# Performance work log

Measured on AMD Instinct MI355X. Metric: run time of the kernel, lower is better.

The kernel has to match this reference:

```python
import jax, jax.numpy as jnp
import numpy as np

CODEBOOK_SIZE = 1024
LATENT_DIM = 64
BETA = 0.25
DECAY = 0.99
EPS = 1e-05


def _hadamard(n):
    H = np.array([[1.0]], dtype=np.float32)
    while H.shape[0] < n:
        H = np.kron(H, np.array([[1.0, 1.0], [1.0, -1.0]], dtype=np.float32))
    return H


def setup_inputs() -> dict:
    key = jax.random.key(0)
    k1, k2, k3 = jax.random.split(key, 3)
    x = jax.random.normal(k1, (16, LATENT_DIM, 64, 64), dtype=jnp.float32)
    lim = 1.0 / CODEBOOK_SIZE
    embedding_weight = jax.random.uniform(k2, (CODEBOOK_SIZE, LATENT_DIM), jnp.float32, -lim, lim)
    ema_w = jax.random.uniform(k3, (CODEBOOK_SIZE, LATENT_DIM), jnp.float32, -lim, lim)
    ema_cluster_size = jnp.ones((CODEBOOK_SIZE,), jnp.float32)
    rotation_matrix = jnp.asarray(_hadamard(LATENT_DIM))
    return {"x": x, "embedding_weight": embedding_weight, "rotation_matrix": rotation_matrix,
            "ema_cluster_size": ema_cluster_size, "ema_w": ema_w}


def reference(x, embedding_weight, rotation_matrix, ema_cluster_size, ema_w):
    sg = jax.lax.stop_gradient
    B, C, H, W = x.shape
    K, D = embedding_weight.shape
    # [B,C,H,W] -> [N, D]
    x_flat = jnp.transpose(x, (0, 2, 3, 1)).reshape(-1, D)
    x_rot = x_flat @ rotation_matrix
    # squared euclidean distances [N, K]
    dist = (jnp.sum(x_rot * x_rot, axis=-1, keepdims=True)
            + jnp.sum(embedding_weight * embedding_weight, axis=-1)[None, :]
            - 2.0 * (x_rot @ embedding_weight.T))
    idx = jnp.argmin(dist, axis=-1)  # [N]
    quant_flat = embedding_weight[idx]  # gather == one-hot @ E
    quant = jnp.transpose(quant_flat.reshape(B, H, W, C), (0, 3, 1, 2))
    commitment_loss = BETA * jnp.mean((sg(quant) - x) ** 2)
    codebook_loss = jnp.mean((quant - sg(x)) ** 2)
    N = x_flat.shape[0]
    counts = jax.ops.segment_sum(jnp.ones((N,), x.dtype), idx, num_segments=K)
    avg_probs = counts / N
    entropy_loss = -jnp.sum(avg_probs * jnp.log(avg_probs + 1e-10))
    loss = codebook_loss + commitment_loss + entropy_loss
    # EMA bookkeeping (training path; detached in the original)
    new_cs = ema_cluster_size * DECAY + (1.0 - DECAY) * counts
    n_tot = jnp.sum(new_cs)
    new_cs = (new_cs + EPS) / (n_tot + K * EPS) * n_tot
    dw = jax.ops.segment_sum(sg(x_rot), idx, num_segments=K)  # encodings.T @ x_rot
    new_ema_w = ema_w * DECAY + (1.0 - DECAY) * dw
    new_embedding = new_ema_w / new_cs[:, None]
    # straight-through estimator
    quant_out = x + sg(quant - x)
    return quant_out, loss, idx, new_embedding, new_cs, new_ema_w
```

## Files before the change

### kernel.cpp

```cpp
#include <hip/hip_runtime.h>
#include <cmath>

#define PAD 68


__global__ __launch_bounds__(256) void vq_init_kernel(const float* __restrict__ E,
                                                      float* __restrict__ ws) {
    #pragma clang fp contract(off)
    int g = blockIdx.x * 256 + threadIdx.x;
    ws[2048 + g] = 0.0f;
    if (g < 1024) {
        ws[1024 + g] = 0.0f;
        const float* e = E + g * 64;
        float r[8];
        #pragma unroll
        for (int j = 0; j < 8; ++j) r[j] = e[j] * e[j];
        #pragma unroll
        for (int t = 1; t < 8; ++t)
            #pragma unroll
            for (int j = 0; j < 8; ++j) {
                float sq = e[8 * t + j] * e[8 * t + j];
                r[j] = r[j] + sq;
            }
        ws[g] = ((r[0] + r[1]) + (r[2] + r[3])) + ((r[4] + r[5]) + (r[6] + r[7]));
    }
    if (g == 0) ws[67584] = 0.0f;
}

__global__ __launch_bounds__(256, 4) void vq_main_kernel(
    const float* __restrict__ x, const float* __restrict__ E,
    const float* __restrict__ R, float* __restrict__ ws, float* __restrict__ out)
{
    #pragma clang fp contract(off)
    __shared__ float s_A[64][PAD];
    __shared__ float s_B[64][PAD];
    __shared__ float s_ee[64];
    __shared__ float s_xx[64];
    __shared__ int   s_idx[64];
    __shared__ float s_red[8];

    const int tid = threadIdx.x;
    const int tc = tid >> 4;
    const int tr = tid & 15;
    const int brow = blockIdx.x;
    const int b = brow >> 6, h = brow & 63;

    const float* ee_g  = ws;
    float* counts  = ws + 1024;
    float* dw      = ws + 2048;
    float* mse_acc = ws + 67584;
    float* out_q   = out;
    float* out_idx = out + 4194305;

    const size_t xbase = (size_t)b * 262144 + (size_t)h * 64;

    #pragma unroll
    for (int i = 0; i < 4; ++i) {
        int d  = i * 16 + (tid >> 4);
        int w4 = (tid & 15) * 4;
        float4 v = *(const float4*)(x + xbase + (size_t)d * 4096 + w4);
        *(float4*)&s_A[d][w4] = v;
        float4 r = *(const float4*)(R + d * 64 + w4);
        *(float4*)&s_B[d][w4] = r;
    }
    __syncthreads();

    {
        float acc[4][4] = {};
        for (int d = 0; d < 64; ++d) {
            float xv[4], rv[4];
            #pragma unroll
            for (int i = 0; i < 4; ++i) xv[i] = s_A[d][tc + 16 * i];
            #pragma unroll
            for (int j = 0; j < 4; ++j) rv[j] = s_B[d][tr + 16 * j];
            #pragma unroll
            for (int i = 0; i < 4; ++i)
                #pragma unroll
                for (int j = 0; j < 4; ++j)
                    acc[i][j] = fmaf(xv[i], rv[j], acc[i][j]);
        }
        __syncthreads();
        #pragma unroll
        for (int i = 0; i < 4; ++i)
            #pragma unroll
            for (int j = 0; j < 4; ++j)
                s_B[tc + 16 * i][tr + 16 * j] = acc[i][j];
    }
    __syncthreads();

    if (tid < 64) {
        const int w = tid;
        float r[8];
        #pragma unroll
        for (int j = 0; j < 8; ++j) { float u = s_B[w][j]; r[j] = u * u; }
        #pragma unroll
        for (int t = 1; t < 8; ++t)
            #pragma unroll
            for (int j = 0; j < 8; ++j) {
                float u = s_B[w][8 * t + j];
                float sq = u * u;
                r[j] = r[j] + sq;
            }
        s_xx[w] = ((r[0] + r[1]) + (r[2] + r[3])) + ((r[4] + r[5]) + (r[6] + r[7]));
    }
    __syncthreads();

    float xxw[4];
    #pragma unroll
    for (int i = 0; i < 4; ++i) xxw[i] = s_xx[tc + 16 * i];

    float bestv[4]; int besti[4];
    #pragma unroll
    for (int i = 0; i < 4; ++i) { bestv[i] = 3.402823466e38f; besti[i] = 0; }

    for (int ch = 0; ch < 16; ++ch) {
        const int c0 = ch * 64;
        #pragma unroll
        for (int i = 0; i < 4; ++i) {
            int f = i * 256 + tid;
            int c = f >> 4, d4 = (f & 15) * 4;
            float4 v = *(const float4*)(E + (size_t)(c0 + c) * 64 + d4);
            *(float4*)&s_A[c][d4] = v;
        }
        if (tid < 64) s_ee[tid] = ee_g[c0 + tid];
        __syncthreads();

        float acc[4][4] = {};
        #pragma unroll
        for (int dq = 0; dq < 16; ++dq) {
            float4 xv[4], ev[4];
            #pragma unroll
            for (int i = 0; i < 4; ++i) xv[i] = *(const float4*)&s_B[tc + 16 * i][dq * 4];
            #pragma unroll
            for (int j = 0; j < 4; ++j) ev[j] = *(const float4*)&s_A[tr + 16 * j][dq * 4];
            #pragma unroll
            for (int i = 0; i < 4; ++i)
                #pragma unroll
                for (int j = 0; j < 4; ++j)
                    acc[i][j] = fmaf(xv[i].x, ev[j].x, acc[i][j]);
            #pragma unroll
            for (int i = 0; i < 4; ++i)
                #pragma unroll
                for (int j = 0; j < 4; ++j)
                    acc[i][j] = fmaf(xv[i].y, ev[j].y, acc[i][j]);
            #pragma unroll
            for (int i = 0; i < 4; ++i)
                #pragma unroll
                for (int j = 0; j < 4; ++j)
                    acc[i][j] = fmaf(xv[i].z, ev[j].z, acc[i][j]);
            #pragma unroll
            for (int i = 0; i < 4; ++i)
                #pragma unroll
                for (int j = 0; j < 4; ++j)
                    acc[i][j] = fmaf(xv[i].w, ev[j].w, acc[i][j]);
        }
        #pragma unroll
        for (int j = 0; j < 4; ++j) {
            int c = c0 + tr + 16 * j;
            float eec = s_ee[tr + 16 * j];
            #pragma unroll
            for (int i = 0; i < 4; ++i) {
                float d1 = xxw[i] + eec;
                float m2 = 2.0f * acc[i][j];
                float dist = d1 - m2;
                if (dist < bestv[i]) { bestv[i] = dist; besti[i] = c; }
            }
        }
        __syncthreads();
    }

    #pragma unroll
    for (int i = 0; i < 4; ++i) {
        float v = bestv[i]; int ix = besti[i];
        #pragma unroll
        for (int m = 1; m < 16; m <<= 1) {
            float ov = __shfl_xor(v, m, 64);
            int   oi = __shfl_xor(ix, m, 64);
            if (ov < v || (ov == v && oi < ix)) { v = ov; ix = oi; }
        }
        const int w = tc + 16 * i;
        if (tr == 0) {
            s_idx[w] = ix;
            out_idx[brow * 64 + w] = (float)ix;
            unsafeAtomicAdd(&counts[ix], 1.0f);
        }
        float4 xr = *(const float4*)&s_B[w][tr * 4];
        float* dst = dw + (size_t)ix * 64 + tr * 4;
        unsafeAtomicAdd(dst + 0, xr.x);
        unsafeAtomicAdd(dst + 1, xr.y);
        unsafeAtomicAdd(dst + 2, xr.z);
        unsafeAtomicAdd(dst + 3, xr.w);
    }
    __syncthreads();

    {
        int w = tid >> 2, p = (tid & 3) * 16;
        int ix = s_idx[w];
        const float* erow = E + (size_t)ix * 64 + p;
        float4 a  = *(const float4*)(erow + 0);
        float4 b4 = *(const float4*)(erow + 4);
        float4 c4 = *(const float4*)(erow + 8);
        float4 d4 = *(const float4*)(erow + 12);
        *(float4*)&s_A[w][p + 0]  = a;
        *(float4*)&s_A[w][p + 4]  = b4;
        *(float4*)&s_A[w][p + 8]  = c4;
        *(float4*)&s_A[w][p + 12] = d4;
    }
    __syncthreads();

    float mse = 0.0f;
    #pragma unroll
    for (int i = 0; i < 4; ++i) {
        int d  = i * 16 + (tid >> 4);
        int w4 = (tid & 15) * 4;
        float4 xv = *(const float4*)(x + xbase + (size_t)d * 4096 + w4);
        float q0 = s_A[w4 + 0][d], q1 = s_A[w4 + 1][d];
        float q2 = s_A[w4 + 2][d], q3 = s_A[w4 + 3][d];
        float4 o;
        o.x = xv.x + (q0 - xv.x);
        o.y = xv.y + (q1 - xv.y);
        o.z = xv.z + (q2 - xv.z);
        o.w = xv.w + (q3 - xv.w);
        float dx = q0 - xv.x, dy = q1 - xv.y, dz = q2 - xv.z, dv = q3 - xv.w;
        mse = fmaf(dx, dx, mse); mse = fmaf(dy, dy, mse);
        mse = fmaf(dz, dz, mse); mse = fmaf(dv, dv, mse);
        *(float4*)(out_q + xbase + (size_t)d * 4096 + w4) = o;
    }
    #pragma unroll
    for (int off = 32; off > 0; off >>= 1) mse += __shfl_down(mse, off, 64);
    int wave = tid >> 6, lane = tid & 63;
    if (lane == 0) s_red[wave] = mse;
    __syncthreads();
    if (tid == 0)
        unsafeAtomicAdd(mse_acc, s_red[0] + s_red[1] + s_red[2] + s_red[3]);
}

__global__ __launch_bounds__(1024) void vq_reduce_kernel(
    const float* __restrict__ ema_cs, float* __restrict__ ws, float* __restrict__ out)
{
    __shared__ float s_red[32];
    const int t = threadIdx.x;
    const float* counts = ws + 1024;
    const float  mse    = ws[67584];

    float cnt = counts[t];
    float p   = cnt * (1.0f / 65536.0f);
    float ent = -p * logf(p + 1e-10f);
    float ncs = ema_cs[t] * 0.99f + 0.01f * cnt;

    float a = ncs, e2 = ent;
    #pragma unroll
    for (int off = 32; off > 0; off >>= 1) {
        a  += __shfl_down(a,  off, 64);
        e2 += __shfl_down(e2, off, 64);
    }
    const int wave = t >> 6;
    if ((t & 63) == 0) { s_red[wave] = a; s_red[16 + wave] = e2; }
    __syncthreads();
    if (t == 0) {
        float sa = 0.0f, se = 0.0f;
        for (int i = 0; i < 16; ++i) { sa += s_red[i]; se += s_red[16 + i]; }
        s_red[0] = sa; s_red[16] = se;
    }
    __syncthreads();
    const float n_tot = s_red[0], ent_tot = s_red[16];

    float ncs_s = (ncs + 1e-5f) / (n_tot + 1024.0f * 1e-5f) * n_tot;
    out[4325377 + t] = ncs_s;
    if (t == 0) {
        out[4194304] = 1.25f * (mse * (1.0f / 4194304.0f)) + ent_tot;
        ws[67585] = n_tot;
    }
}

__global__ __launch_bounds__(256) void vq_update_kernel(
    const float* __restrict__ ema_cs, const float* __restrict__ ema_w,
    const float* __restrict__ ws, float* __restrict__ out)
{
    __shared__ float s_inv[64];
    const int t = threadIdx.x;
    const int base_code = blockIdx.x * 64;
    const float* counts = ws + 1024;
    const float* dw     = ws + 2048;
    const float  n_tot  = ws[67585];

    if (t < 64) {
        int code = base_code + t;
        float ncs = ema_cs[code] * 0.99f + 0.01f * counts[code];
        float ncs_s = (ncs + 1e-5f) / (n_tot + 1024.0f * 1e-5f) * n_tot;
        s_inv[t] = 1.0f / ncs_s;
    }
    __syncthreads();

    float* out_emb  = out + 4259841;
    float* out_emaw = out + 4326401;
    const int base_e = base_code * 64;

    #pragma unroll
    for (int k = 0; k < 16; ++k) {
        int el = k * 256 + t;
        int e  = base_e + el;
        float nw = ema_w[e] * 0.99f + 0.01f * dw[e];
        out_emaw[e] = nw;
        out_emb[e]  = nw * s_inv[el >> 6];
    }
}

extern "C" void kernel_launch(void* const* d_in, const int* in_sizes, int n_in,
                              void* d_out, int out_size, void* d_ws, size_t ws_size,
                              hipStream_t stream) {
    const float* x      = (const float*)d_in[0];
    const float* E      = (const float*)d_in[1];
    const float* R      = (const float*)d_in[2];
    const float* ema_cs = (const float*)d_in[3];
    const float* ema_w  = (const float*)d_in[4];
    float* out = (float*)d_out;
    float* ws  = (float*)d_ws;

    hipLaunchKernelGGL(vq_init_kernel,   dim3(256),  dim3(256),  0, stream, E, ws);
    hipLaunchKernelGGL(vq_main_kernel,   dim3(1024), dim3(256),  0, stream, x, E, R, ws, out);
    hipLaunchKernelGGL(vq_reduce_kernel, dim3(1),    dim3(1024), 0, stream, ema_cs, ws, out);
    hipLaunchKernelGGL(vq_update_kernel, dim3(16),   dim3(256),  0, stream, ema_cs, ema_w, ws, out);
}
```

Before: 251.9 us.

## Enlarge distance tile to 128x128 per block and merge reduce/update kernels

Each block of the main kernel now handles two image rows (128 vectors) and processes the codebook in 128-code chunks with an 8x8 register tile per thread. This raises arithmetic intensity and halves the grid size, reducing how often the codebook is reloaded into shared memory. Occupancy is lowered to 2 blocks per CU and register pressure rises. The separate single-block reduce kernel and the update kernel are merged into one 17-block final kernel in which each block recomputes n_tot, removing one launch and one serial dependency.

```diff
diff --git a/kernel.cpp b/kernel.cpp
--- a/kernel.cpp
+++ b/kernel.cpp
@@ -1,7 +1,5 @@
 #include <hip/hip_runtime.h>
 #include <cmath>
-
-#define PAD 68
 
 
 __global__ __launch_bounds__(256) void vq_init_kernel(const float* __restrict__ E,
@@ -27,23 +25,23 @@
     if (g == 0) ws[67584] = 0.0f;
 }
 
-__global__ __launch_bounds__(256, 4) void vq_main_kernel(
+__global__ __launch_bounds__(256, 2) void vq_main_kernel(
     const float* __restrict__ x, const float* __restrict__ E,
     const float* __restrict__ R, float* __restrict__ ws, float* __restrict__ out)
 {
     #pragma clang fp contract(off)
-    __shared__ float s_A[64][PAD];
-    __shared__ float s_B[64][PAD];
-    __shared__ float s_ee[64];
-    __shared__ float s_xx[64];
-    __shared__ int   s_idx[64];
+    __shared__ float s_A[8704];
+    __shared__ float s_B[8704];
+    __shared__ float s_ee[128];
+    __shared__ float s_xx[128];
+    __shared__ int   s_idx[128];
     __shared__ float s_red[8];
 
     const int tid = threadIdx.x;
-    const int tc = tid >> 4;
-    const int tr = tid & 15;
+    const int tg = tid >> 4;
+    const int cg = tid & 15;
     const int brow = blockIdx.x;
-    const int b = brow >> 6, h = brow & 63;
+    const int b = brow >> 5, hp = brow & 31;
 
     const float* ee_g  = ws;
     float* counts  = ws + 1024;
@@ -52,52 +50,55 @@
     float* out_q   = out;
     float* out_idx = out + 4194305;
 
-    const size_t xbase = (size_t)b * 262144 + (size_t)h * 64;
-
+    const size_t xbase = (size_t)b * 262144 + (size_t)hp * 128;
+
+    #pragma unroll
+    for (int i = 0; i < 8; ++i) {
+        int d  = i * 8 + (tid >> 5);
+        int t4 = (tid & 31) * 4;
+        *(float4*)&s_A[d * 132 + t4] = *(const float4*)(x + xbase + (size_t)d * 4096 + t4);
+    }
     #pragma unroll
     for (int i = 0; i < 4; ++i) {
         int d  = i * 16 + (tid >> 4);
-        int w4 = (tid & 15) * 4;
-        float4 v = *(const float4*)(x + xbase + (size_t)d * 4096 + w4);
-        *(float4*)&s_A[d][w4] = v;
-        float4 r = *(const float4*)(R + d * 64 + w4);
-        *(float4*)&s_B[d][w4] = r;
+        int j4 = (tid & 15) * 4;
+        *(float4*)&s_B[d * 68 + j4] = *(const float4*)(R + d * 64 + j4);
     }
     __syncthreads();
 
     {
-        float acc[4][4] = {};
+        float acc[8][4] = {};
         for (int d = 0; d < 64; ++d) {
-            float xv[4], rv[4];
-            #pragma unroll
-            for (int i = 0; i < 4; ++i) xv[i] = s_A[d][tc + 16 * i];
-            #pragma unroll
-            for (int j = 0; j < 4; ++j) rv[j] = s_B[d][tr + 16 * j];
-            #pragma unroll
-            for (int i = 0; i < 4; ++i)
-                #pragma unroll
-                for (int j = 0; j < 4; ++j)
-                    acc[i][j] = fmaf(xv[i], rv[j], acc[i][j]);
-        }
-        __syncthreads();
-        #pragma unroll
-        for (int i = 0; i < 4; ++i)
-            #pragma unroll
-            for (int j = 0; j < 4; ++j)
-                s_B[tc + 16 * i][tr + 16 * j] = acc[i][j];
-    }
-    __syncthreads();
-
-    if (tid < 64) {
+            float xv[8], rv[4];
+            #pragma unroll
+            for (int i = 0; i < 8; ++i) xv[i] = s_A[d * 132 + tg + 16 * i];
+            #pragma unroll
+            for (int jj = 0; jj < 4; ++jj) rv[jj] = s_B[d * 68 + cg + 16 * jj];
+            #pragma unroll
+            for (int i = 0; i < 8; ++i)
+                #pragma unroll
+                for (int jj = 0; jj < 4; ++jj)
+                    acc[i][jj] = fmaf(xv[i], rv[jj], acc[i][jj]);
+        }
+        __syncthreads();
+        #pragma unroll
+        for (int i = 0; i < 8; ++i)
+            #pragma unroll
+            for (int jj = 0; jj < 4; ++jj)
+                s_B[(tg + 16 * i) * 68 + cg + 16 * jj] = acc[i][jj];
+    }
+    __syncthreads();
+
+    if (tid < 128) {
         const int w = tid;
         float r[8];
         #pragma unroll
-        for (int j = 0; j < 8; ++j) { float u = s_B[w][j]; r[j] = u * u; }
+        for (int j = 0; j < 8; ++j) { float u = s_B[w * 68 + j]; r[j] = u * u; }
         #pragma unroll
         for (int t = 1; t < 8; ++t)
             #pragma unroll
             for (int j = 0; j < 8; ++j) {
-                float u = s_B[w][8 * t + j];
+                float u = s_B[w * 68 + 8 * t + j];
                 float sq = u * u;
                 r[j] = r[j] + sq;
             }
@@ -105,61 +106,60 @@
     }
     __syncthreads();
 
-    float xxw[4];
-    #pragma unroll
-    for (int i = 0; i < 4; ++i) xxw[i] = s_xx[tc + 16 * i];
-
-    float bestv[4]; int besti[4];
-    #pragma unroll
-    for (int i = 0; i < 4; ++i) { bestv[i] = 3.402823466e38f; besti[i] = 0; }
-
-    for (int ch = 0; ch < 16; ++ch) {
-        const int c0 = ch * 64;
-        #pragma unroll
-        for (int i = 0; i < 4; ++i) {
-            int f = i * 256 + tid;
+    float xxw[8];
+    #pragma unroll
+    for (int i = 0; i < 8; ++i) xxw[i] = s_xx[tg + 16 * i];
+
+    float bestv[8]; int besti[8];
+    #pragma unroll
+    for (int i = 0; i < 8; ++i) { bestv[i] = 3.402823466e38f; besti[i] = 0; }
+
+    for (int pc = 0; pc < 8; ++pc) {
+        const int c0 = pc * 128;
+        #pragma unroll
+        for (int it = 0; it < 8; ++it) {
+            int f = it * 256 + tid;
             int c = f >> 4, d4 = (f & 15) * 4;
-            float4 v = *(const float4*)(E + (size_t)(c0 + c) * 64 + d4);
-            *(float4*)&s_A[c][d4] = v;
-        }
-        if (tid < 64) s_ee[tid] = ee_g[c0 + tid];
-        __syncthreads();
-
-        float acc[4][4] = {};
-        #pragma unroll
+            *(float4*)&s_A[c * 68 + d4] = *(const float4*)(E + (size_t)(c0 + c) * 64 + d4);
+        }
+        if (tid < 128) s_ee[tid] = ee_g[c0 + tid];
+        __syncthreads();
+
+        float acc[8][8] = {};
+        #pragma unroll 4
         for (int dq = 0; dq < 16; ++dq) {
-            float4 xv[4], ev[4];
-            #pragma unroll
-            for (int i = 0; i < 4; ++i) xv[i] = *(const float4*)&s_B[tc + 16 * i][dq * 4];
-            #pragma unroll
-            for (int j = 0; j < 4; ++j) ev[j] = *(const float4*)&s_A[tr + 16 * j][dq * 4];
-            #pragma unroll
-            for (int i = 0; i < 4; ++i)
-                #pragma unroll
-                for (int j = 0; j < 4; ++j)
+            float4 xv[8], ev[8];
+            #pragma unroll
+            for (int i = 0; i < 8; ++i) xv[i] = *(const float4*)&s_B[(tg + 16 * i) * 68 + dq * 4];
+            #pragma unroll
+            for (int j = 0; j < 8; ++j) ev[j] = *(const float4*)&s_A[(cg + 16 * j) * 68 + dq * 4];
+            #pragma unroll
+            for (int i = 0; i < 8; ++i)
+                #pragma unroll
+                for (int j = 0; j < 8; ++j)
                     acc[i][j] = fmaf(xv[i].x, ev[j].x, acc[i][j]);
             #pragma unroll
-            for (int i = 0; i < 4; ++i)
-                #pragma unroll
-                for (int j = 0; j < 4; ++j)
+            for (int i = 0; i < 8; ++i)
+                #pragma unroll
+                for (int j = 0; j < 8; ++j)
                     acc[i][j] = fmaf(xv[i].y, ev[j].y, acc[i][j]);
             #pragma unroll
-            for (int i = 0; i < 4; ++i)
-                #pragma unroll
-                for (int j = 0; j < 4; ++j)
+            for (int i = 0; i < 8; ++i)
+                #pragma unroll
+                for (int j = 0; j < 8; ++j)
                     acc[i][j] = fmaf(xv[i].z, ev[j].z, acc[i][j]);
             #pragma unroll
-            for (int i = 0; i < 4; ++i)
-                #pragma unroll
-                for (int j = 0; j < 4; ++j)
+            for (int i = 0; i < 8; ++i)
+                #pragma unroll
+                for (int j = 0; j < 8; ++j)
                     acc[i][j] = fmaf(xv[i].w, ev[j].w, acc[i][j]);
         }
         #pragma unroll
-        for (int j = 0; j < 4; ++j) {
-            int c = c0 + tr + 16 * j;
-            float eec = s_ee[tr + 16 * j];
-            #pragma unroll
-            for (int i = 0; i < 4; ++i) {
+        for (int j = 0; j < 8; ++j) {
+            int c = c0 + cg + 16 * j;
+            float eec = s_ee[cg + 16 * j];
+            #pragma unroll
+            for (int i = 0; i < 8; ++i) {
                 float d1 = xxw[i] + eec;
                 float m2 = 2.0f * acc[i][j];
                 float dist = d1 - m2;
@@ -170,7 +170,7 @@
     }
 
     #pragma unroll
-    for (int i = 0; i < 4; ++i) {
+    for (int i = 0; i < 8; ++i) {
         float v = bestv[i]; int ix = besti[i];
         #pragma unroll
         for (int m = 1; m < 16; m <<= 1) {
@@ -178,14 +178,14 @@
             int   oi = __shfl_xor(ix, m, 64);
             if (ov < v || (ov == v && oi < ix)) { v = ov; ix = oi; }
         }
-        const int w = tc + 16 * i;
-        if (tr == 0) {
+        const int w = tg + 16 * i;
+        if (cg == 0) {
             s_idx[w] = ix;
-            out_idx[brow * 64 + w] = (float)ix;
+            out_idx[brow * 128 + w] = (float)ix;
             unsafeAtomicAdd(&counts[ix], 1.0f);
         }
-        float4 xr = *(const float4*)&s_B[w][tr * 4];
-        float* dst = dw + (size_t)ix * 64 + tr * 4;
+        float4 xr = *(const float4*)&s_B[w * 68 + cg * 4];
+        float* dst = dw + (size_t)ix * 64 + cg * 4;
         unsafeAtomicAdd(dst + 0, xr.x);
         unsafeAtomicAdd(dst + 1, xr.y);
         unsafeAtomicAdd(dst + 2, xr.z);
@@ -194,37 +194,29 @@
     __syncthreads();
 
     {
-        int w = tid >> 2, p = (tid & 3) * 16;
+        int w = tid >> 1, p = (tid & 1) * 32;
         int ix = s_idx[w];
         const float* erow = E + (size_t)ix * 64 + p;
-        float4 a  = *(const float4*)(erow + 0);
-        float4 b4 = *(const float4*)(erow + 4);
-        float4 c4 = *(const float4*)(erow + 8);
-        float4 d4 = *(const float4*)(erow + 12);
-        *(float4*)&s_A[w][p + 0]  = a;
-        *(float4*)&s_A[w][p + 4]  = b4;
-        *(float4*)&s_A[w][p + 8]  = c4;
-        *(float4*)&s_A[w][p + 12] = d4;
+        #pragma unroll
+        for (int k = 0; k < 8; ++k)
+            *(float4*)&s_A[w * 68 + p + 4 * k] = *(const float4*)(erow + 4 * k);
     }
     __syncthreads();
 
     float mse = 0.0f;
     #pragma unroll
-    for (int i = 0; i < 4; ++i) {
-        int d  = i * 16 + (tid >> 4);
-        int w4 = (tid & 15) * 4;
-        float4 xv = *(const float4*)(x + xbase + (size_t)d * 4096 + w4);
-        float q0 = s_A[w4 + 0][d], q1 = s_A[w4 + 1][d];
-        float q2 = s_A[w4 + 2][d], q3 = s_A[w4 + 3][d];
-        float4 o;
-        o.x = xv.x + (q0 - xv.x);
-        o.y = xv.y + (q1 - xv.y);
-        o.z = xv.z + (q2 - xv.z);
-        o.w = xv.w + (q3 - xv.w);
-        float dx = q0 - xv.x, dy = q1 - xv.y, dz = q2 - xv.z, dv = q3 - xv.w;
-        mse = fmaf(dx, dx, mse); mse = fmaf(dy, dy, mse);
-        mse = fmaf(dz, dz, mse); mse = fmaf(dv, dv, mse);
-        *(float4*)(out_q + xbase + (size_t)d * 4096 + w4) = o;
+    for (int i = 0; i < 8; ++i) {
+        int d = i * 8 + (tid >> 5);
+        #pragma unroll
+        for (int k = 0; k < 4; ++k) {
+            int t = (tid & 31) + 32 * k;
+            float xv = x[xbase + (size_t)d * 4096 + t];
+            float q  = s_A[t * 68 + d];
+            float o  = xv + (q - xv);
+            float df = q - xv;
+            mse = fmaf(df, df, mse);
+            out_q[xbase + (size_t)d * 4096 + t] = o;
+        }
     }
     #pragma unroll
     for (int off = 32; off > 0; off >>= 1) mse += __shfl_down(mse, off, 64);
@@ -235,74 +227,70 @@
         unsafeAtomicAdd(mse_acc, s_red[0] + s_red[1] + s_red[2] + s_red[3]);
 }
 
-__global__ __launch_bounds__(1024) void vq_reduce_kernel(
-    const float* __restrict__ ema_cs, float* __restrict__ ws, float* __restrict__ out)
-{
-    __shared__ float s_red[32];
-    const int t = threadIdx.x;
-    const float* counts = ws + 1024;
-    const float  mse    = ws[67584];
-
-    float cnt = counts[t];
-    float p   = cnt * (1.0f / 65536.0f);
-    float ent = -p * logf(p + 1e-10f);
-    float ncs = ema_cs[t] * 0.99f + 0.01f * cnt;
-
-    float a = ncs, e2 = ent;
-    #pragma unroll
-    for (int off = 32; off > 0; off >>= 1) {
-        a  += __shfl_down(a,  off, 64);
-        e2 += __shfl_down(e2, off, 64);
-    }
-    const int wave = t >> 6;
-    if ((t & 63) == 0) { s_red[wave] = a; s_red[16 + wave] = e2; }
-    __syncthreads();
-    if (t == 0) {
-        float sa = 0.0f, se = 0.0f;
-        for (int i = 0; i < 16; ++i) { sa += s_red[i]; se += s_red[16 + i]; }
-        s_red[0] = sa; s_red[16] = se;
-    }
-    __syncthreads();
-    const float n_tot = s_red[0], ent_tot = s_red[16];
-
-    float ncs_s = (ncs + 1e-5f) / (n_tot + 1024.0f * 1e-5f) * n_tot;
-    out[4325377 + t] = ncs_s;
-    if (t == 0) {
-        out[4194304] = 1.25f * (mse * (1.0f / 4194304.0f)) + ent_tot;
-        ws[67585] = n_tot;
-    }
-}
-
-__global__ __launch_bounds__(256) void vq_update_kernel(
+__global__ __launch_bounds__(256) void vq_final_kernel(
     const float* __restrict__ ema_cs, const float* __restrict__ ema_w,
     const float* __restrict__ ws, float* __restrict__ out)
 {
+    __shared__ float s_red[8];
     __shared__ float s_inv[64];
     const int t = threadIdx.x;
-    const int base_code = blockIdx.x * 64;
+    const int bid = blockIdx.x;
     const float* counts = ws + 1024;
     const float* dw     = ws + 2048;
-    const float  n_tot  = ws[67585];
-
-    if (t < 64) {
-        int code = base_code + t;
-        float ncs = ema_cs[code] * 0.99f + 0.01f * counts[code];
-        float ncs_s = (ncs + 1e-5f) / (n_tot + 1024.0f * 1e-5f) * n_tot;
-        s_inv[t] = 1.0f / ncs_s;
-    }
-    __syncthreads();
-
-    float* out_emb  = out + 4259841;
-    float* out_emaw = out + 4326401;
-    const int base_e = base_code * 64;
-
-    #pragma unroll
-    for (int k = 0; k < 16; ++k) {
-        int el = k * 256 + t;
-        int e  = base_e + el;
-        float nw = ema_w[e] * 0.99f + 0.01f * dw[e];
-        out_emaw[e] = nw;
-        out_emb[e]  = nw * s_inv[el >> 6];
+
+    float part = 0.0f;
+    #pragma unroll
+    for (int k = 0; k < 4; ++k) {
+        int c = k * 256 + t;
+        part += ema_cs[c] * 0.99f + 0.01f * counts[c];
+    }
+    #pragma unroll
+    for (int off = 32; off > 0; off >>= 1) part += __shfl_down(part, off, 64);
+    if ((t & 63) == 0) s_red[t >> 6] = part;
+    __syncthreads();
+    const float n_tot = s_red[0] + s_red[1] + s_red[2] + s_red[3];
+    const float denom = n_tot + 1024.0f * 1e-5f;
+
+    if (bid < 16) {
+        const int base_code = bid * 64;
+        if (t < 64) {
+            int code = base_code + t;
+            float ncs = ema_cs[code] * 0.99f + 0.01f * counts[code];
+            float ncs_s = (ncs + 1e-5f) / denom * n_tot;
+            s_inv[t] = 1.0f / ncs_s;
+        }
+        __syncthreads();
+        float* out_emb  = out + 4259841;
+        float* out_emaw = out + 4326401;
+        const int base_e = base_code * 64;
+        #pragma unroll
+        for (int k = 0; k < 16; ++k) {
+            int el = k * 256 + t;
+            int e  = base_e + el;
+            float nw = ema_w[e] * 0.99f + 0.01f * dw[e];
+            out_emaw[e] = nw;
+            out_emb[e]  = nw * s_inv[el >> 6];
+        }
+    } else {
+        float ent_part = 0.0f;
+        #pragma unroll
+        for (int k = 0; k < 4; ++k) {
+            int c = k * 256 + t;
+            float cnt = counts[c];
+            float p   = cnt * (1.0f / 65536.0f);
+            ent_part += -p * logf(p + 1e-10f);
+            float ncs = ema_cs[c] * 0.99f + 0.01f * cnt;
+            out[4325377 + c] = (ncs + 1e-5f) / denom * n_tot;
+        }
+        __syncthreads();
+        #pragma unroll
+        for (int off = 32; off > 0; off >>= 1) ent_part += __shfl_down(ent_part, off, 64);
+        if ((t & 63) == 0) s_red[t >> 6] = ent_part;
+        __syncthreads();
+        if (t == 0) {
+            float ent_tot = s_red[0] + s_red[1] + s_red[2] + s_red[3];
+            out[4194304] = 1.25f * (ws[67584] * (1.0f / 4194304.0f)) + ent_tot;
+        }
     }
 }
 
@@ -317,8 +305,7 @@
     float* out = (float*)d_out;
     float* ws  = (float*)d_ws;
 
-    hipLaunchKernelGGL(vq_init_kernel,   dim3(256),  dim3(256),  0, stream, E, ws);
-    hipLaunchKernelGGL(vq_main_kernel,   dim3(1024), dim3(256),  0, stream, x, E, R, ws, out);
-    hipLaunchKernelGGL(vq_reduce_kernel, dim3(1),    dim3(1024), 0, stream, ema_cs, ws, out);
-    hipLaunchKernelGGL(vq_update_kernel, dim3(16),   dim3(256),  0, stream, ema_cs, ema_w, ws, out);
+    hipLaunchKernelGGL(vq_init_kernel,  dim3(256), dim3(256), 0, stream, E, ws);
+    hipLaunchKernelGGL(vq_main_kernel,  dim3(512), dim3(256), 0, stream, x, E, R, ws, out);
+    hipLaunchKernelGGL(vq_final_kernel, dim3(17),  dim3(256), 0, stream, ema_cs, ema_w, ws, out);
 }
```

Result: slower. 271.4 us (+7.8%).
